# Kernel optimization log

Hardware: AMD Instinct MI355X
Metric: run time of the kernel (lower is better)

Reference implementation:

```python
import jax, jax.numpy as jnp
import numpy as np

BS = 128      # batch
L = 512       # encoder sequence length
ENC = 512     # enc_hs
DEC = 1024    # dec_hs
ATTN = 512    # attn_sz
EMB = 256     # emb_sz
VOCAB = 128   # alphabet_size
MAX_LEN = 128 # text_max_len
SOS = 0


def setup_inputs() -> dict:
    key = jax.random.key(0)
    ks = jax.random.split(key, 10)
    s = 0.02
    return {
        "enc_out": jax.random.normal(ks[0], (BS, ENC, L), jnp.float32),
        # attention.encoder_conv (Conv1d enc->attn, kernel 1 == matmul)
        "W_enc": jax.random.normal(ks[1], (ATTN, ENC), jnp.float32) * s,
        "b_enc": jnp.zeros((ATTN,), jnp.float32),
        # attention.decoder_linear
        "W_dec": jax.random.normal(ks[2], (ATTN, DEC), jnp.float32) * s,
        "b_dec": jnp.zeros((ATTN,), jnp.float32),
        # attention.energy_layer (Conv1d attn->1, kernel 1)
        "v_e": jax.random.normal(ks[3], (ATTN,), jnp.float32) * s,
        "b_e": jnp.zeros((), jnp.float32),
        # embedding table
        "emb_table": jax.random.normal(ks[4], (VOCAB, EMB), jnp.float32) * s,
        # LSTM (single layer), PyTorch gate order i,f,g,o
        "W_ih": jax.random.normal(ks[5], (4 * DEC, EMB + ENC), jnp.float32) * s,
        "W_hh": jax.random.normal(ks[6], (4 * DEC, DEC), jnp.float32) * s,
        "b_ih": jnp.zeros((4 * DEC,), jnp.float32),
        "b_hh": jnp.zeros((4 * DEC,), jnp.float32),
        # output projection
        "W_out": jax.random.normal(ks[7], (VOCAB, DEC), jnp.float32) * s,
        "b_out": jnp.zeros((VOCAB,), jnp.float32),
    }


def reference(enc_out, W_enc, b_enc, W_dec, b_dec, v_e, b_e, emb_table,
              W_ih, W_hh, b_ih, b_hh, W_out, b_out):
    bs = enc_out.shape[0]
    # encoder_conv applied once: [bs, attn, L]
    weighted_enc = jnp.einsum('ae,bel->bal', W_enc, enc_out) + b_enc[None, :, None]

    def step(carry, _):
        x_idx, h, c = carry
        emb_x = emb_table[x_idx]                                   # [bs, emb]
        # Bahdanau attention
        wdec = h @ W_dec.T + b_dec                                 # [bs, attn]
        pre = jnp.tanh(weighted_enc + wdec[:, :, None])            # [bs, attn, L]
        scores = jnp.einsum('bal,a->bl', pre, v_e) + b_e           # [bs, L]
        alphas = jax.nn.softmax(scores, axis=-1)                   # [bs, L]
        context = jnp.einsum('bel,bl->be', enc_out, alphas)        # [bs, enc]
        # LSTM cell (PyTorch gate order i, f, g, o)
        rnn_x = jnp.concatenate([emb_x, context], axis=1)          # [bs, emb+enc]
        gates = rnn_x @ W_ih.T + b_ih + h @ W_hh.T + b_hh          # [bs, 4*dec]
        i, f, g, o = jnp.split(gates, 4, axis=1)
        i = jax.nn.sigmoid(i); f = jax.nn.sigmoid(f)
        g = jnp.tanh(g); o = jax.nn.sigmoid(o)
        c_new = f * c + i * g
        h_new = o * jnp.tanh(c_new)
        logits = h_new @ W_out.T + b_out                           # [bs, vocab]
        logp = jax.nn.log_softmax(logits, axis=-1)
        next_word = jnp.argmax(logp, axis=1).astype(jnp.int32)
        return (next_word, h_new, c_new), (logp, next_word, alphas)

    x0 = jnp.full((bs,), SOS, dtype=jnp.int32)
    h0 = jnp.zeros((bs, DEC), enc_out.dtype)
    c0 = jnp.zeros((bs, DEC), enc_out.dtype)
    _, (logp, preds, attn) = jax.lax.scan(step, (x0, h0, c0), None, length=MAX_LEN)
    # [T,bs,*] -> [bs,T,*]
    return logp.transpose(1, 0, 2), preds.transpose(1, 0), attn.transpose(1, 0, 2)
```

## Files before the change

### kernel.cpp

```cpp
#include <hip/hip_runtime.h>
#include <math.h>

#define BS 128
#define L 512
#define ENC 512
#define DEC 1024
#define ATTN 512
#define EMB 256
#define VOCAB 128
#define TMAX 128
#define KCAT 1792
#define G4 4096

#define OFF_WET    0ull
#define OFF_WGR    33554432ull
#define OFF_BGR    40894464ull
#define OFF_WOUTT  40898560ull
#define OFF_WDT    41029632ull
#define OFF_C      41553920ull
#define OFF_WDEC   41684992ull
#define OFF_SC     41750528ull
#define OFF_XCAT   41816064ull
#define OFF_GPART  42045440ull

__device__ __forceinline__ float tanh_fast(float x) {
    float ax = fabsf(x);
    float e = __expf(-2.f * ax);
    float d = 1.f + e;
    float r = __builtin_amdgcn_rcpf(d);
    r = r * (2.f - d * r);
    float t = 1.f - 2.f * e * r;
    return copysignf(t, x);
}

__global__ void k_prep(const float* __restrict__ W_ih, const float* __restrict__ W_hh,
                       const float* __restrict__ b_ih, const float* __restrict__ b_hh,
                       const float* __restrict__ W_out, const float* __restrict__ W_dec,
                       float* __restrict__ Wgr, float* __restrict__ bgr,
                       float* __restrict__ WoutT, float* __restrict__ WdT) {
    long i = (long)blockIdx.x * 256 + threadIdx.x;
    if (i < (long)G4 * KCAT) {
        int mp = (int)(i / KCAT), k = (int)(i % KCAT);
        int d = mp >> 2, g = mp & 3;
        int r = g * DEC + d;
        Wgr[i] = (k < EMB + ENC) ? W_ih[(long)r * (EMB + ENC) + k]
                                 : W_hh[(long)r * DEC + (k - (EMB + ENC))];
        return;
    }
    long j = i - (long)G4 * KCAT;
    if (j < G4) {
        int d = (int)(j >> 2), g = (int)(j & 3);
        int r = g * DEC + d;
        bgr[j] = b_ih[r] + b_hh[r];
        return;
    }
    long m = j - G4;
    if (m < (long)DEC * VOCAB) {
        int k = (int)(m / VOCAB), v = (int)(m % VOCAB);
        WoutT[m] = W_out[(long)v * DEC + k];
        return;
    }
    long p = m - (long)DEC * VOCAB;
    if (p < (long)DEC * ATTN) {
        int k = (int)(p / ATTN), a = (int)(p % ATTN);
        WdT[p] = W_dec[(long)a * DEC + k];
    }
}

__global__ void k_init(const float* __restrict__ emb_table, const float* __restrict__ b_dec,
                       float* __restrict__ c, float* __restrict__ Xcat,
                       float* __restrict__ wdec) {
    long i = (long)blockIdx.x * 256 + threadIdx.x;
    if (i < BS * DEC) { c[i] = 0.f; return; }
    long j = i - BS * DEC;
    if (j < (long)BS * KCAT) {
        int cdx = (int)(j % KCAT);
        Xcat[j] = (cdx < EMB) ? emb_table[cdx] : 0.f;
        return;
    }
    long p = j - (long)BS * KCAT;
    if (p < (long)BS * ATTN) {
        wdec[p] = b_dec[(int)(p % ATTN)];
    }
}

__global__ __launch_bounds__(256) void k_wenc(const float* __restrict__ W_enc,
                                              const float* __restrict__ b_enc,
                                              const float* __restrict__ enc_out,
                                              float* __restrict__ weT) {
    __shared__ float As[16][68];
    __shared__ float Bs[16][68];
    int b = blockIdx.z;
    int a0 = blockIdx.y * 64;
    int l0 = blockIdx.x * 64;
    int t = threadIdx.x;
    int ty = t >> 4, tx = t & 15;
    float acc[4][4] = {};
    for (int e0 = 0; e0 < ENC; e0 += 16) {
        {
            int ar = t >> 2;
            int kg = (t & 3) << 2;
            float4 w4 = *(const float4*)&W_enc[(size_t)(a0 + ar) * ENC + e0 + kg];
            As[kg + 0][ar] = w4.x; As[kg + 1][ar] = w4.y; As[kg + 2][ar] = w4.z; As[kg + 3][ar] = w4.w;
            int er = t >> 4;
            int lg = (t & 15) << 2;
            float4 x4 = *(const float4*)&enc_out[((size_t)b * ENC + e0 + er) * L + l0 + lg];
            *(float4*)&Bs[er][lg] = x4;
        }
        __syncthreads();
        #pragma unroll
        for (int kk = 0; kk < 16; kk++) {
            float4 a4 = *(const float4*)&As[kk][ty * 4];
            float4 x4 = *(const float4*)&Bs[kk][tx * 4];
            float av[4] = {a4.x, a4.y, a4.z, a4.w};
            float xv[4] = {x4.x, x4.y, x4.z, x4.w};
            #pragma unroll
            for (int i = 0; i < 4; i++)
                #pragma unroll
                for (int j = 0; j < 4; j++) acc[i][j] += av[i] * xv[j];
        }
        __syncthreads();
    }
    float be0 = b_enc[a0 + ty * 4 + 0];
    float be1 = b_enc[a0 + ty * 4 + 1];
    float be2 = b_enc[a0 + ty * 4 + 2];
    float be3 = b_enc[a0 + ty * 4 + 3];
    #pragma unroll
    for (int j = 0; j < 4; j++) {
        int l = l0 + tx * 4 + j;
        float4 o = {acc[0][j] + be0, acc[1][j] + be1, acc[2][j] + be2, acc[3][j] + be3};
        *(float4*)&weT[((size_t)b * L + l) * ATTN + a0 + ty * 4] = o;
    }
}

__global__ __launch_bounds__(512) void k_attn(const float* __restrict__ weT,
                                              const float* __restrict__ wdec,
                                              const float* __restrict__ v_e,
                                              const float* __restrict__ b_e,
                                              const float* __restrict__ enc_out,
                                              float* __restrict__ attn_out,
                                              float* __restrict__ Xcat, int t_step) {
    __shared__ float wd[ATTN];
    __shared__ float ve[ATTN];
    __shared__ float al[L];
    __shared__ float red[512];
    int b = blockIdx.x;
    int t = threadIdx.x;
    wd[t] = wdec[(size_t)b * ATTN + t];
    ve[t] = v_e[t];
    __syncthreads();
    const float* row = weT + ((size_t)b * L + t) * ATTN;
    float acc = 0.f;
    #pragma unroll 8
    for (int a4 = 0; a4 < ATTN; a4 += 4) {
        float4 x = *(const float4*)&row[a4];
        acc += ve[a4 + 0] * tanh_fast(x.x + wd[a4 + 0]);
        acc += ve[a4 + 1] * tanh_fast(x.y + wd[a4 + 1]);
        acc += ve[a4 + 2] * tanh_fast(x.z + wd[a4 + 2]);
        acc += ve[a4 + 3] * tanh_fast(x.w + wd[a4 + 3]);
    }
    float sc = acc + b_e[0];
    red[t] = sc;
    __syncthreads();
    for (int s = 256; s; s >>= 1) { if (t < s) red[t] = fmaxf(red[t], red[t + s]); __syncthreads(); }
    float m = red[0];
    __syncthreads();
    float e = expf(sc - m);
    red[t] = e;
    __syncthreads();
    for (int s = 256; s; s >>= 1) { if (t < s) red[t] += red[t + s]; __syncthreads(); }
    float inv = 1.f / red[0];
    al[t] = e * inv;
    __syncthreads();
    attn_out[((size_t)b * TMAX + t_step) * L + t] = al[t];
    const float* erow = enc_out + ((size_t)b * ENC + t) * L;
    float cacc = 0.f;
    #pragma unroll 8
    for (int l4 = 0; l4 < L; l4 += 4) {
        float4 x = *(const float4*)&erow[l4];
        float4 a4 = *(const float4*)&al[l4];
        cacc += x.x * a4.x + x.y * a4.y + x.z * a4.z + x.w * a4.w;
    }
    Xcat[(size_t)b * KCAT + EMB + t] = cacc;
}

__global__ __launch_bounds__(256) void k_gates(const float* __restrict__ Wgr,
                                               const float* __restrict__ Xcat,
                                               float* __restrict__ gates_part) {
    __shared__ float As[16][68];
    __shared__ float Xs[16][68];
    int M0 = blockIdx.x * 64;
    int b0 = blockIdx.y * 64;
    int ks = blockIdx.z;
    int kbase = ks * 448, kend = kbase + 448;
    int t = threadIdx.x, ty = t >> 4, tx = t & 15;
    int r = t >> 2, kg = (t & 3) << 2;
    float acc[4][4] = {};
    float4 wreg = *(const float4*)&Wgr[(size_t)(M0 + r) * KCAT + kbase + kg];
    float4 xreg = *(const float4*)&Xcat[(size_t)(b0 + r) * KCAT + kbase + kg];
    for (int k0 = kbase; k0 < kend; k0 += 16) {
        As[kg + 0][r] = wreg.x; As[kg + 1][r] = wreg.y; As[kg + 2][r] = wreg.z; As[kg + 3][r] = wreg.w;
        Xs[kg + 0][r] = xreg.x; Xs[kg + 1][r] = xreg.y; Xs[kg + 2][r] = xreg.z; Xs[kg + 3][r] = xreg.w;
        __syncthreads();
        if (k0 + 16 < kend) {
            wreg = *(const float4*)&Wgr[(size_t)(M0 + r) * KCAT + k0 + 16 + kg];
            xreg = *(const float4*)&Xcat[(size_t)(b0 + r) * KCAT + k0 + 16 + kg];
        }
        #pragma unroll
        for (int kk = 0; kk < 16; kk++) {
            float4 a4 = *(const float4*)&As[kk][ty * 4];
            float4 x4 = *(const float4*)&Xs[kk][tx * 4];
            float av[4] = {a4.x, a4.y, a4.z, a4.w};
            float xv[4] = {x4.x, x4.y, x4.z, x4.w};
            #pragma unroll
            for (int i = 0; i < 4; i++)
                #pragma unroll
                for (int j = 0; j < 4; j++) acc[i][j] += av[i] * xv[j];
        }
        __syncthreads();
    }
    float* gp = gates_part + (size_t)ks * BS * G4;
    #pragma unroll
    for (int j = 0; j < 4; j++) {
        float4 o = {acc[0][j], acc[1][j], acc[2][j], acc[3][j]};
        *(float4*)&gp[(size_t)(b0 + tx * 4 + j) * G4 + M0 + ty * 4] = o;
    }
}

__global__ __launch_bounds__(512) void k_out_cell(const float* __restrict__ gates_part,
                                                  const float* __restrict__ bgr,
                                                  const float* __restrict__ WoutT,
                                                  const float* __restrict__ b_out,
                                                  const float* __restrict__ emb_table,
                                                  const float* __restrict__ WdT,
                                                  const float* __restrict__ b_dec,
                                                  float* __restrict__ c,
                                                  float* __restrict__ logp_out,
                                                  float* __restrict__ preds_out,
                                                  float* __restrict__ Xcat,
                                                  float* __restrict__ wdec, int t_step) {
    __shared__ float hs[DEC];
    __shared__ float red[512];
    __shared__ float rv[128];
    __shared__ int ri[128];
    int b = blockIdx.x;
    int t = threadIdx.x;
    #pragma unroll
    for (int q = 0; q < 2; q++) {
        int d = q * 512 + t;
        const float* gp = gates_part + (size_t)b * G4 + d * 4;
        float4 g = *(const float4*)gp;
        #pragma unroll
        for (int ks = 1; ks < 4; ks++) {
            float4 p = *(const float4*)(gp + (size_t)ks * BS * G4);
            g.x += p.x; g.y += p.y; g.z += p.z; g.w += p.w;
        }
        float4 bb = *(const float4*)&bgr[(size_t)d * 4];
        float gi = g.x + bb.x, gf = g.y + bb.y, gg = g.z + bb.z, go = g.w + bb.w;
        float fi = 1.f / (1.f + expf(-gi));
        float ff = 1.f / (1.f + expf(-gf));
        float fg = tanhf(gg);
        float fo = 1.f / (1.f + expf(-go));
        size_t ix = (size_t)b * DEC + d;
        float cn = ff * c[ix] + fi * fg;
        float hn = fo * tanhf(cn);
        c[ix] = cn;
        hs[d] = hn;
        Xcat[(size_t)b * KCAT + EMB + ENC + d] = hn;
    }
    __syncthreads();
    int v = t & 127, kh = t >> 7;
    const float* wp = WoutT + (size_t)kh * 256 * VOCAB + v;
    float acc = 0.f;
    #pragma unroll 8
    for (int k = 0; k < 256; k++) acc += wp[(size_t)k * VOCAB] * hs[kh * 256 + k];
    red[t] = acc;
    __syncthreads();
    float logits = 0.f;
    if (t < 128) {
        logits = ((red[t] + red[t + 128]) + (red[t + 256] + red[t + 384])) + b_out[t];
        rv[t] = logits; ri[t] = t;
    }
    __syncthreads();
    for (int s = 64; s; s >>= 1) {
        if (t < s) {
            float ov = rv[t + s]; int oi = ri[t + s];
            if (ov > rv[t] || (ov == rv[t] && oi < ri[t])) { rv[t] = ov; ri[t] = oi; }
        }
        __syncthreads();
    }
    float m = rv[0]; int am = ri[0];
    __syncthreads();
    if (t < 128) red[t] = expf(logits - m);
    __syncthreads();
    for (int s = 64; s; s >>= 1) { if (t < s && t + s < 128) red[t] += red[t + s]; __syncthreads(); }
    if (t < 128) logp_out[((size_t)b * TMAX + t_step) * VOCAB + t] = logits - m - logf(red[0]);
    if (t == 0) preds_out[(size_t)b * TMAX + t_step] = (float)am;
    if (t < 256) Xcat[(size_t)b * KCAT + t] = emb_table[(size_t)am * EMB + t];
    {
        const float* wdp = WdT + t;
        float s = 0.f;
        #pragma unroll 16
        for (int k = 0; k < DEC; k++) s += wdp[(size_t)k * ATTN] * hs[k];
        wdec[(size_t)b * ATTN + t] = s + b_dec[t];
    }
}

extern "C" void kernel_launch(void* const* d_in, const int* in_sizes, int n_in,
                              void* d_out, int out_size, void* d_ws, size_t ws_size,
                              hipStream_t stream) {
    const float* enc_out = (const float*)d_in[0];
    const float* W_enc   = (const float*)d_in[1];
    const float* b_enc   = (const float*)d_in[2];
    const float* W_dec   = (const float*)d_in[3];
    const float* b_dec   = (const float*)d_in[4];
    const float* v_e     = (const float*)d_in[5];
    const float* b_e     = (const float*)d_in[6];
    const float* emb     = (const float*)d_in[7];
    const float* W_ih    = (const float*)d_in[8];
    const float* W_hh    = (const float*)d_in[9];
    const float* b_ih    = (const float*)d_in[10];
    const float* b_hh    = (const float*)d_in[11];
    const float* W_out   = (const float*)d_in[12];
    const float* b_out   = (const float*)d_in[13];

    float* ws    = (float*)d_ws;
    float* weT   = ws + OFF_WET;
    float* Wgr   = ws + OFF_WGR;
    float* bgr   = ws + OFF_BGR;
    float* WoutT = ws + OFF_WOUTT;
    float* WdT   = ws + OFF_WDT;
    float* c     = ws + OFF_C;
    float* wdec  = ws + OFF_WDEC;
    float* Xcat  = ws + OFF_XCAT;
    float* gpart = ws + OFF_GPART;

    float* logp_out  = (float*)d_out;
    float* preds_out = logp_out + (size_t)BS * TMAX * VOCAB;
    float* attn_out  = preds_out + (size_t)BS * TMAX;

    {
        long n = (long)G4 * KCAT + G4 + (long)DEC * VOCAB + (long)DEC * ATTN;
        k_prep<<<(int)((n + 255) / 256), 256, 0, stream>>>(W_ih, W_hh, b_ih, b_hh, W_out, W_dec,
                                                           Wgr, bgr, WoutT, WdT);
    }
    {
        long n = (long)BS * DEC + (long)BS * KCAT + (long)BS * ATTN;
        k_init<<<(int)((n + 255) / 256), 256, 0, stream>>>(emb, b_dec, c, Xcat, wdec);
    }
    k_wenc<<<dim3(8, 8, 128), 256, 0, stream>>>(W_enc, b_enc, enc_out, weT);

    for (int t = 0; t < TMAX; t++) {
        k_attn<<<128, 512, 0, stream>>>(weT, wdec, v_e, b_e, enc_out, attn_out, Xcat, t);
        k_gates<<<dim3(64, 2, 4), 256, 0, stream>>>(Wgr, Xcat, gpart);
        k_out_cell<<<128, 512, 0, stream>>>(gpart, bgr, WoutT, b_out, emb, WdT, b_dec,
                                            c, logp_out, preds_out, Xcat, wdec, t);
    }
}
```

Before: 21.28 ms.

## Fuse LSTM cell/output step with next attention step; halve gates batch tile

```diff
diff --git a/kernel.cpp b/kernel.cpp
--- a/kernel.cpp
+++ b/kernel.cpp
@@ -18,8 +18,6 @@
 #define OFF_WOUTT  40898560ull
 #define OFF_WDT    41029632ull
 #define OFF_C      41553920ull
-#define OFF_WDEC   41684992ull
-#define OFF_SC     41750528ull
 #define OFF_XCAT   41816064ull
 #define OFF_GPART  42045440ull
 
@@ -67,20 +65,14 @@
     }
 }
 
-__global__ void k_init(const float* __restrict__ emb_table, const float* __restrict__ b_dec,
-                       float* __restrict__ c, float* __restrict__ Xcat,
-                       float* __restrict__ wdec) {
+__global__ void k_init(const float* __restrict__ emb_table,
+                       float* __restrict__ c, float* __restrict__ Xcat) {
     long i = (long)blockIdx.x * 256 + threadIdx.x;
     if (i < BS * DEC) { c[i] = 0.f; return; }
     long j = i - BS * DEC;
     if (j < (long)BS * KCAT) {
         int cdx = (int)(j % KCAT);
         Xcat[j] = (cdx < EMB) ? emb_table[cdx] : 0.f;
-        return;
-    }
-    long p = j - (long)BS * KCAT;
-    if (p < (long)BS * ATTN) {
-        wdec[p] = b_dec[(int)(p % ATTN)];
     }
 }
 
@@ -133,22 +125,99 @@
     }
 }
 
-__global__ __launch_bounds__(512) void k_attn(const float* __restrict__ weT,
-                                              const float* __restrict__ wdec,
-                                              const float* __restrict__ v_e,
-                                              const float* __restrict__ b_e,
-                                              const float* __restrict__ enc_out,
-                                              float* __restrict__ attn_out,
-                                              float* __restrict__ Xcat, int t_step) {
+__global__ __launch_bounds__(512) void k_ao(const float* __restrict__ gpart,
+                                            const float* __restrict__ bgr,
+                                            const float* __restrict__ WoutT,
+                                            const float* __restrict__ b_out,
+                                            const float* __restrict__ emb_table,
+                                            const float* __restrict__ WdT,
+                                            const float* __restrict__ b_dec,
+                                            float* __restrict__ c,
+                                            float* __restrict__ logp_out,
+                                            float* __restrict__ preds_out,
+                                            float* __restrict__ Xcat,
+                                            const float* __restrict__ weT,
+                                            const float* __restrict__ v_e,
+                                            const float* __restrict__ b_e,
+                                            const float* __restrict__ enc_out,
+                                            float* __restrict__ attn_out, int ts) {
+    __shared__ float hs[DEC];
     __shared__ float wd[ATTN];
     __shared__ float ve[ATTN];
     __shared__ float al[L];
     __shared__ float red[512];
+    __shared__ float rv[128];
+    __shared__ int ri[128];
     int b = blockIdx.x;
     int t = threadIdx.x;
-    wd[t] = wdec[(size_t)b * ATTN + t];
+
+    if (ts > 0) {
+        #pragma unroll
+        for (int q = 0; q < 2; q++) {
+            int d = q * 512 + t;
+            const float* gp = gpart + (size_t)b * G4 + d * 4;
+            float4 g = *(const float4*)gp;
+            #pragma unroll
+            for (int ks = 1; ks < 4; ks++) {
+                float4 p = *(const float4*)(gp + (size_t)ks * BS * G4);
+                g.x += p.x; g.y += p.y; g.z += p.z; g.w += p.w;
+            }
+            float4 bb = *(const float4*)&bgr[(size_t)d * 4];
+            float gi = g.x + bb.x, gf = g.y + bb.y, gg = g.z + bb.z, go = g.w + bb.w;
+            float fi = 1.f / (1.f + expf(-gi));
+            float ff = 1.f / (1.f + expf(-gf));
+            float fg = tanhf(gg);
+            float fo = 1.f / (1.f + expf(-go));
+            size_t ix = (size_t)b * DEC + d;
+            float cn = ff * c[ix] + fi * fg;
+            float hn = fo * tanhf(cn);
+            c[ix] = cn;
+            hs[d] = hn;
+            Xcat[(size_t)b * KCAT + EMB + ENC + d] = hn;
+        }
+        __syncthreads();
+        int v = t & 127, kh = t >> 7;
+        const float* wp = WoutT + (size_t)kh * 256 * VOCAB + v;
+        float acc = 0.f;
+        #pragma unroll 8
+        for (int k = 0; k < 256; k++) acc += wp[(size_t)k * VOCAB] * hs[kh * 256 + k];
+        red[t] = acc;
+        __syncthreads();
+        float logits = 0.f;
+        if (t < 128) {
+            logits = ((red[t] + red[t + 128]) + (red[t + 256] + red[t + 384])) + b_out[t];
+            rv[t] = logits; ri[t] = t;
+        }
+        __syncthreads();
+        for (int s = 64; s; s >>= 1) {
+            if (t < s) {
+                float ov = rv[t + s]; int oi = ri[t + s];
+                if (ov > rv[t] || (ov == rv[t] && oi < ri[t])) { rv[t] = ov; ri[t] = oi; }
+            }
+            __syncthreads();
+        }
+        float m = rv[0]; int am = ri[0];
+        __syncthreads();
+        if (t < 128) red[t] = expf(logits - m);
+        __syncthreads();
+        for (int s = 64; s; s >>= 1) { if (t < s && t + s < 128) red[t] += red[t + s]; __syncthreads(); }
+        if (t < 128) logp_out[((size_t)b * TMAX + (ts - 1)) * VOCAB + t] = logits - m - logf(red[0]);
+        if (t == 0) preds_out[(size_t)b * TMAX + (ts - 1)] = (float)am;
+        if (t < 256) Xcat[(size_t)b * KCAT + t] = emb_table[(size_t)am * EMB + t];
+        {
+            const float* wdp = WdT + t;
+            float s = 0.f;
+            #pragma unroll 16
+            for (int k = 0; k < DEC; k++) s += wdp[(size_t)k * ATTN] * hs[k];
+            wd[t] = s + b_dec[t];
+        }
+        if (ts == TMAX) return;
+    } else {
+        wd[t] = b_dec[t];
+    }
     ve[t] = v_e[t];
     __syncthreads();
+
     const float* row = weT + ((size_t)b * L + t) * ATTN;
     float acc = 0.f;
     #pragma unroll 8
@@ -172,7 +241,7 @@
     float inv = 1.f / red[0];
     al[t] = e * inv;
     __syncthreads();
-    attn_out[((size_t)b * TMAX + t_step) * L + t] = al[t];
+    attn_out[((size_t)b * TMAX + ts) * L + t] = al[t];
     const float* erow = enc_out + ((size_t)b * ENC + t) * L;
     float cacc = 0.f;
     #pragma unroll 8
@@ -188,121 +257,43 @@
                                                const float* __restrict__ Xcat,
                                                float* __restrict__ gates_part) {
     __shared__ float As[16][68];
-    __shared__ float Xs[16][68];
+    __shared__ float Xs[16][36];
     int M0 = blockIdx.x * 64;
-    int b0 = blockIdx.y * 64;
+    int b0 = blockIdx.y * 32;
     int ks = blockIdx.z;
     int kbase = ks * 448, kend = kbase + 448;
     int t = threadIdx.x, ty = t >> 4, tx = t & 15;
     int r = t >> 2, kg = (t & 3) << 2;
-    float acc[4][4] = {};
+    float acc[4][2] = {};
     float4 wreg = *(const float4*)&Wgr[(size_t)(M0 + r) * KCAT + kbase + kg];
-    float4 xreg = *(const float4*)&Xcat[(size_t)(b0 + r) * KCAT + kbase + kg];
+    float4 xreg;
+    if (t < 128) xreg = *(const float4*)&Xcat[(size_t)(b0 + r) * KCAT + kbase + kg];
     for (int k0 = kbase; k0 < kend; k0 += 16) {
         As[kg + 0][r] = wreg.x; As[kg + 1][r] = wreg.y; As[kg + 2][r] = wreg.z; As[kg + 3][r] = wreg.w;
-        Xs[kg + 0][r] = xreg.x; Xs[kg + 1][r] = xreg.y; Xs[kg + 2][r] = xreg.z; Xs[kg + 3][r] = xreg.w;
+        if (t < 128) {
+            Xs[kg + 0][r] = xreg.x; Xs[kg + 1][r] = xreg.y; Xs[kg + 2][r] = xreg.z; Xs[kg + 3][r] = xreg.w;
+        }
         __syncthreads();
         if (k0 + 16 < kend) {
             wreg = *(const float4*)&Wgr[(size_t)(M0 + r) * KCAT + k0 + 16 + kg];
-            xreg = *(const float4*)&Xcat[(size_t)(b0 + r) * KCAT + k0 + 16 + kg];
+            if (t < 128) xreg = *(const float4*)&Xcat[(size_t)(b0 + r) * KCAT + k0 + 16 + kg];
         }
         #pragma unroll
         for (int kk = 0; kk < 16; kk++) {
             float4 a4 = *(const float4*)&As[kk][ty * 4];
-            float4 x4 = *(const float4*)&Xs[kk][tx * 4];
-            float av[4] = {a4.x, a4.y, a4.z, a4.w};
-            float xv[4] = {x4.x, x4.y, x4.z, x4.w};
-            #pragma unroll
-            for (int i = 0; i < 4; i++)
-                #pragma unroll
-                for (int j = 0; j < 4; j++) acc[i][j] += av[i] * xv[j];
+            float xb0 = Xs[kk][tx * 2], xb1 = Xs[kk][tx * 2 + 1];
+            acc[0][0] += a4.x * xb0; acc[0][1] += a4.x * xb1;
+            acc[1][0] += a4.y * xb0; acc[1][1] += a4.y * xb1;
+            acc[2][0] += a4.z * xb0; acc[2][1] += a4.z * xb1;
+            acc[3][0] += a4.w * xb0; acc[3][1] += a4.w * xb1;
         }
         __syncthreads();
     }
     float* gp = gates_part + (size_t)ks * BS * G4;
     #pragma unroll
-    for (int j = 0; j < 4; j++) {
+    for (int j = 0; j < 2; j++) {
         float4 o = {acc[0][j], acc[1][j], acc[2][j], acc[3][j]};
-        *(float4*)&gp[(size_t)(b0 + tx * 4 + j) * G4 + M0 + ty * 4] = o;
-    }
-}
-
-__global__ __launch_bounds__(512) void k_out_cell(const float* __restrict__ gates_part,
-                                                  const float* __restrict__ bgr,
-                                                  const float* __restrict__ WoutT,
-                                                  const float* __restrict__ b_out,
-                                                  const float* __restrict__ emb_table,
-                                                  const float* __restrict__ WdT,
-                                                  const float* __restrict__ b_dec,
-                                                  float* __restrict__ c,
-                                                  float* __restrict__ logp_out,
-                                                  float* __restrict__ preds_out,
-                                                  float* __restrict__ Xcat,
-                                                  float* __restrict__ wdec, int t_step) {
-    __shared__ float hs[DEC];
-    __shared__ float red[512];
-    __shared__ float rv[128];
-    __shared__ int ri[128];
-    int b = blockIdx.x;
-    int t = threadIdx.x;
-    #pragma unroll
-    for (int q = 0; q < 2; q++) {
-        int d = q * 512 + t;
-        const float* gp = gates_part + (size_t)b * G4 + d * 4;
-        float4 g = *(const float4*)gp;
-        #pragma unroll
-        for (int ks = 1; ks < 4; ks++) {
-            float4 p = *(const float4*)(gp + (size_t)ks * BS * G4);
-            g.x += p.x; g.y += p.y; g.z += p.z; g.w += p.w;
-        }
-        float4 bb = *(const float4*)&bgr[(size_t)d * 4];
-        float gi = g.x + bb.x, gf = g.y + bb.y, gg = g.z + bb.z, go = g.w + bb.w;
-        float fi = 1.f / (1.f + expf(-gi));
-        float ff = 1.f / (1.f + expf(-gf));
-        float fg = tanhf(gg);
-        float fo = 1.f / (1.f + expf(-go));
-        size_t ix = (size_t)b * DEC + d;
-        float cn = ff * c[ix] + fi * fg;
-        float hn = fo * tanhf(cn);
-        c[ix] = cn;
-        hs[d] = hn;
-        Xcat[(size_t)b * KCAT + EMB + ENC + d] = hn;
-    }
-    __syncthreads();
-    int v = t & 127, kh = t >> 7;
-    const float* wp = WoutT + (size_t)kh * 256 * VOCAB + v;
-    float acc = 0.f;
-    #pragma unroll 8
-    for (int k = 0; k < 256; k++) acc += wp[(size_t)k * VOCAB] * hs[kh * 256 + k];
-    red[t] = acc;
-    __syncthreads();
-    float logits = 0.f;
-    if (t < 128) {
-        logits = ((red[t] + red[t + 128]) + (red[t + 256] + red[t + 384])) + b_out[t];
-        rv[t] = logits; ri[t] = t;
-    }
-    __syncthreads();
-    for (int s = 64; s; s >>= 1) {
-        if (t < s) {
-            float ov = rv[t + s]; int oi = ri[t + s];
-            if (ov > rv[t] || (ov == rv[t] && oi < ri[t])) { rv[t] = ov; ri[t] = oi; }
-        }
-        __syncthreads();
-    }
-    float m = rv[0]; int am = ri[0];
-    __syncthreads();
-    if (t < 128) red[t] = expf(logits - m);
-    __syncthreads();
-    for (int s = 64; s; s >>= 1) { if (t < s && t + s < 128) red[t] += red[t + s]; __syncthreads(); }
-    if (t < 128) logp_out[((size_t)b * TMAX + t_step) * VOCAB + t] = logits - m - logf(red[0]);
-    if (t == 0) preds_out[(size_t)b * TMAX + t_step] = (float)am;
-    if (t < 256) Xcat[(size_t)b * KCAT + t] = emb_table[(size_t)am * EMB + t];
-    {
-        const float* wdp = WdT + t;
-        float s = 0.f;
-        #pragma unroll 16
-        for (int k = 0; k < DEC; k++) s += wdp[(size_t)k * ATTN] * hs[k];
-        wdec[(size_t)b * ATTN + t] = s + b_dec[t];
+        *(float4*)&gp[(size_t)(b0 + tx * 2 + j) * G4 + M0 + ty * 4] = o;
     }
 }
 
@@ -331,7 +322,6 @@
     float* WoutT = ws + OFF_WOUTT;
     float* WdT   = ws + OFF_WDT;
     float* c     = ws + OFF_C;
-    float* wdec  = ws + OFF_WDEC;
     float* Xcat  = ws + OFF_XCAT;
     float* gpart = ws + OFF_GPART;
 
@@ -345,15 +335,18 @@
                                                            Wgr, bgr, WoutT, WdT);
     }
     {
-        long n = (long)BS * DEC + (long)BS * KCAT + (long)BS * ATTN;
-        k_init<<<(int)((n + 255) / 256), 256, 0, stream>>>(emb, b_dec, c, Xcat, wdec);
+        long n = (long)BS * DEC + (long)BS * KCAT;
+        k_init<<<(int)((n + 255) / 256), 256, 0, stream>>>(emb, c, Xcat);
     }
     k_wenc<<<dim3(8, 8, 128), 256, 0, stream>>>(W_enc, b_enc, enc_out, weT);
 
     for (int t = 0; t < TMAX; t++) {
-        k_attn<<<128, 512, 0, stream>>>(weT, wdec, v_e, b_e, enc_out, attn_out, Xcat, t);
-        k_gates<<<dim3(64, 2, 4), 256, 0, stream>>>(Wgr, Xcat, gpart);
-        k_out_cell<<<128, 512, 0, stream>>>(gpart, bgr, WoutT, b_out, emb, WdT, b_dec,
-                                            c, logp_out, preds_out, Xcat, wdec, t);
-    }
-}
+        k_ao<<<128, 512, 0, stream>>>(gpart, bgr, WoutT, b_out, emb, WdT, b_dec, c,
+                                      logp_out, preds_out, Xcat, weT, v_e, b_e,
+                                      enc_out, attn_out, t);
+        k_gates<<<dim3(64, 4, 4), 256, 0, stream>>>(Wgr, Xcat, gpart);
+    }
+    k_ao<<<128, 512, 0, stream>>>(gpart, bgr, WoutT, b_out, emb, WdT, b_dec, c,
+                                  logp_out, preds_out, Xcat, weT, v_e, b_e,
+                                  enc_out, attn_out, TMAX);
+}
```

Measured after the change: 22.07 ms. +3.7%, slower.
